# Kernel optimization log

Measured on AMD Instinct MI355X. Metric: run time of the kernel, lower is better.

The kernel has to match this reference:

```python
import jax, jax.numpy as jnp
import numpy as np

B, S, D = 4, 2048, 2048
E = 64           # num_experts
TOPK = 2         # num_experts_per_token


def setup_inputs() -> dict:
    key = jax.random.key(0)
    k1, k2, k3 = jax.random.split(key, 3)
    x_real = jax.random.normal(k1, (B, S, D), dtype=jnp.float32)
    x_imag = jax.random.normal(k2, (B, S, D), dtype=jnp.float32)
    # flax Dense: kernel [in_features, out_features] with lecun_normal-ish scale
    W = jax.random.normal(k3, (2 * D, E), dtype=jnp.float32) / np.sqrt(2.0 * D)
    b = jnp.zeros((E,), dtype=jnp.float32)
    return {"x_real": x_real, "x_imag": x_imag, "W": W, "b": b}


def reference(x_real, x_imag, W, b):
    # amp = |x|, phase = angle(x) for x = x_real + i*x_imag
    amp = jnp.hypot(x_real, x_imag)                 # [B,S,D]
    phase = jnp.arctan2(x_imag, x_real)             # [B,S,D]
    routing_input = jnp.concatenate([amp, phase], axis=-1)  # [B,S,2D]
    scores = jnp.einsum('bsf,fe->bse', routing_input, W) + b  # [B,S,E]
    probs = jax.nn.softmax(scores, axis=-1)
    top_k_probs, top_k_indices = jax.lax.top_k(probs, TOPK)   # [B,S,K]
    top_k_probs = top_k_probs / jnp.sum(top_k_probs, axis=-1, keepdims=True)
    return (top_k_probs, top_k_indices)
```

## Files before the change

### kernel.cpp

```cpp
#include <hip/hip_runtime.h>
#include <math.h>

#define NTOK 8192
#define DD   2048
#define EE   64
#define MTILE 32
#define KSPLIT 2
#define DPER (DD/KSPLIT)
#define DCHUNK 32
#define NCHUNK (DPER/DCHUNK)
#define APAD 8
#define ASTRIDE (64 + APAD)
#define PROB_N (NTOK*2)

typedef __bf16 bf16x8 __attribute__((ext_vector_type(8)));
typedef float  f32x4  __attribute__((ext_vector_type(4)));

__device__ __forceinline__ unsigned short bf16_rne(float x, float& rep) {
    unsigned u = __builtin_bit_cast(unsigned, x);
    unsigned r = u + 0x7FFFu + ((u >> 16) & 1u);
    unsigned short h = (unsigned short)(r >> 16);
    rep = __builtin_bit_cast(float, (unsigned)h << 16);
    return h;
}

__device__ __forceinline__ void split3(float x, unsigned short& h1,
                                       unsigned short& h2, unsigned short& h3) {
    float f1, f2, f3;
    h1 = bf16_rne(x, f1);
    float r1 = x - f1;
    h2 = bf16_rne(r1, f2);
    float r2 = r1 - f2;
    h3 = bf16_rne(r2, f3);
}

__global__ __launch_bounds__(256) void wsplit(const float* __restrict__ W,
                                              unsigned short* __restrict__ Wt) {
    const int g  = blockIdx.x * 256 + threadIdx.x;
    const int f  = g >> 4;
    const int e4 = g & 15;
    const float4 w = *((const float4*)(W + (size_t)f * EE) + e4);
    const float v[4] = {w.x, w.y, w.z, w.w};
    #pragma unroll
    for (int j = 0; j < 4; ++j) {
        unsigned short h1, h2, h3;
        split3(v[j], h1, h2, h3);
        const int e = e4 * 4 + j;
        Wt[((size_t)(0 * EE + e)) * 4096 + f] = h1;
        Wt[((size_t)(1 * EE + e)) * 4096 + f] = h2;
        Wt[((size_t)(2 * EE + e)) * 4096 + f] = h3;
    }
}

__global__ __launch_bounds__(256) void gemm_mfma(
    const float* __restrict__ xr, const float* __restrict__ xi,
    const unsigned short* __restrict__ Wt, float* __restrict__ part)
{
    __shared__ __align__(16) unsigned short As[3][MTILE][ASTRIDE];

    const int bid   = blockIdx.x;
    const int ks    = bid & (KSPLIT - 1);
    const int strip = bid >> 1;
    const int t0    = strip * MTILE;
    const int dbase = ks * DPER;

    const int tid  = threadIdx.x;
    const int lane = tid & 63;
    const int wv   = tid >> 6;
    const int n0   = wv * 16;

    const int stok = tid >> 3;
    const int sf4  = tid & 7;

    const int fm = lane & 15;
    const int fq = lane >> 4;

    f32x4 acc[2][3];
    #pragma unroll
    for (int mt = 0; mt < 2; ++mt)
        #pragma unroll
        for (int g = 0; g < 3; ++g)
            acc[mt][g] = (f32x4){0.f, 0.f, 0.f, 0.f};

    const float* prx = xr + (size_t)(t0 + stok) * DD + dbase + 4 * sf4;
    const float* pix = xi + (size_t)(t0 + stok) * DD + dbase + 4 * sf4;
    float4 vr = *(const float4*)prx;
    float4 vi = *(const float4*)pix;

    const unsigned short* wb = Wt + (size_t)(n0 + fm) * 4096 + 8 * fq;

    for (int c = 0; c < NCHUNK; ++c) {
        const int d0 = dbase + c * DCHUNK;

        bf16x8 bfr[2][3];
        #pragma unroll
        for (int s = 0; s < 3; ++s) {
            bfr[0][s] = *(const bf16x8*)(wb + (size_t)s * (EE * 4096) + d0);
            bfr[1][s] = *(const bf16x8*)(wb + (size_t)s * (EE * 4096) + 2048 + d0);
        }
        const int cn = (c + 1 < NCHUNK) ? (c + 1) : c;
        const float4 nvr = *(const float4*)(prx + cn * DCHUNK);
        const float4 nvi = *(const float4*)(pix + cn * DCHUNK);

        {
            const float ar[4] = {vr.x, vr.y, vr.z, vr.w};
            const float ai[4] = {vi.x, vi.y, vi.z, vi.w};
            ushort4 a1, a2, a3, p1, p2, p3;
            unsigned short* pa1 = (unsigned short*)&a1;
            unsigned short* pa2 = (unsigned short*)&a2;
            unsigned short* pa3 = (unsigned short*)&a3;
            unsigned short* pp1 = (unsigned short*)&p1;
            unsigned short* pp2 = (unsigned short*)&p2;
            unsigned short* pp3 = (unsigned short*)&p3;
            #pragma unroll
            for (int j = 0; j < 4; ++j) {
                const float amp = sqrtf(ar[j] * ar[j] + ai[j] * ai[j]);
                const float ph  = atan2f(ai[j], ar[j]);
                split3(amp, pa1[j], pa2[j], pa3[j]);
                split3(ph,  pp1[j], pp2[j], pp3[j]);
            }
            *(ushort4*)&As[0][stok][4 * sf4]      = a1;
            *(ushort4*)&As[1][stok][4 * sf4]      = a2;
            *(ushort4*)&As[2][stok][4 * sf4]      = a3;
            *(ushort4*)&As[0][stok][32 + 4 * sf4] = p1;
            *(ushort4*)&As[1][stok][32 + 4 * sf4] = p2;
            *(ushort4*)&As[2][stok][32 + 4 * sf4] = p3;
        }
        __syncthreads();

        #pragma unroll
        for (int st = 0; st < 2; ++st) {
            #pragma unroll
            for (int mt = 0; mt < 2; ++mt) {
                const unsigned short* ab = &As[0][mt * 16 + fm][st * 32 + fq * 8];
                const bf16x8 a0 = *(const bf16x8*)(ab);
                const bf16x8 a1 = *(const bf16x8*)(ab + MTILE * ASTRIDE);
                const bf16x8 a2 = *(const bf16x8*)(ab + 2 * MTILE * ASTRIDE);
                acc[mt][0] = __builtin_amdgcn_mfma_f32_16x16x32_bf16(a0, bfr[st][0], acc[mt][0], 0, 0, 0);
                acc[mt][0] = __builtin_amdgcn_mfma_f32_16x16x32_bf16(a1, bfr[st][1], acc[mt][0], 0, 0, 0);
                acc[mt][1] = __builtin_amdgcn_mfma_f32_16x16x32_bf16(a0, bfr[st][1], acc[mt][1], 0, 0, 0);
                acc[mt][1] = __builtin_amdgcn_mfma_f32_16x16x32_bf16(a1, bfr[st][0], acc[mt][1], 0, 0, 0);
                acc[mt][2] = __builtin_amdgcn_mfma_f32_16x16x32_bf16(a0, bfr[st][2], acc[mt][2], 0, 0, 0);
                acc[mt][2] = __builtin_amdgcn_mfma_f32_16x16x32_bf16(a2, bfr[st][0], acc[mt][2], 0, 0, 0);
            }
        }
        __syncthreads();
        vr = nvr; vi = nvi;
    }

    #pragma unroll
    for (int mt = 0; mt < 2; ++mt) {
        const f32x4 s = acc[mt][0] + acc[mt][1] + acc[mt][2];
        float* pb = part + ((size_t)ks * NTOK + t0 + mt * 16) * EE;
        #pragma unroll
        for (int r = 0; r < 4; ++r)
            pb[(size_t)(fq * 4 + r) * EE + n0 + fm] = s[r];
    }
}

__global__ __launch_bounds__(256) void finalize_topk(
    const float* __restrict__ part, const float* __restrict__ bias,
    float* __restrict__ out)
{
    const int tid  = threadIdx.x;
    const int lane = tid & 63;
    const int w    = tid >> 6;
    const int t    = blockIdx.x * 4 + w;

    float s = bias[lane];
    #pragma unroll
    for (int p = 0; p < KSPLIT; ++p)
        s += part[((size_t)p * NTOK + t) * EE + lane];

    float v1 = s, v2 = -INFINITY;
    int   i1 = lane, i2 = 64;

    #pragma unroll
    for (int off = 1; off < 64; off <<= 1) {
        const float ov1 = __shfl_xor(v1, off, 64);
        const int   oi1 = __shfl_xor(i1, off, 64);
        const float ov2 = __shfl_xor(v2, off, 64);
        const int   oi2 = __shfl_xor(i2, off, 64);
        const bool b1 = (ov1 > v1) || (ov1 == v1 && oi1 < i1);
        const float n1 = b1 ? ov1 : v1;  const int ni1 = b1 ? oi1 : i1;
        const float c1 = b1 ? v1  : ov1; const int ci1 = b1 ? i1  : oi1;
        const float c2 = b1 ? ov2 : v2;  const int ci2 = b1 ? oi2 : i2;
        const bool b2 = (c1 > c2) || (c1 == c2 && ci1 < ci2);
        v1 = n1; i1 = ni1;
        v2 = b2 ? c1 : c2; i2 = b2 ? ci1 : ci2;
    }

    if (lane == 0) {
        const float z  = expf(v2 - v1);
        const float p1 = 1.0f / (1.0f + z);
        const float p2 = z / (1.0f + z);
        out[(size_t)t * 2 + 0] = p1;
        out[(size_t)t * 2 + 1] = p2;
        out[PROB_N + (size_t)t * 2 + 0] = (float)i1;
        out[PROB_N + (size_t)t * 2 + 1] = (float)i2;
    }
}

extern "C" void kernel_launch(void* const* d_in, const int* in_sizes, int n_in,
                              void* d_out, int out_size, void* d_ws, size_t ws_size,
                              hipStream_t stream) {
    const float* xr = (const float*)d_in[0];
    const float* xi = (const float*)d_in[1];
    const float* W  = (const float*)d_in[2];
    const float* b  = (const float*)d_in[3];
    float* out = (float*)d_out;

    float* part = (float*)d_ws;
    unsigned short* Wt = (unsigned short*)((char*)d_ws + (size_t)KSPLIT * NTOK * EE * 4);

    wsplit<<<256, 256, 0, stream>>>(W, Wt);
    gemm_mfma<<<(NTOK / MTILE) * KSPLIT, 256, 0, stream>>>(xr, xi, Wt, part);
    finalize_topk<<<NTOK / 4, 256, 0, stream>>>(part, b, out);
}
```

Measured before the change: 195.8 us.

## Drop LDS staging, compute A fragments in registers, split-K 4 with atomics

Each wave now loads its own 16 token rows and builds the amp/phase bf16 split fragments directly in registers, which removes the shared-memory staging and both block barriers. The tile grows to 64 tokens with 4 wave-rows, and each wave covers all 64 experts with 4 accumulators. K is split 4 ways and partial scores are combined with float atomicAdd into a buffer that the wsplit kernel zeroes. This removes the LDS round trip and the partial-sum reads in the finalize kernel. In exchange each wave reloads the full W fragment set with no sharing across waves, more register pressure is accepted, and atomic accumulation makes the summation order nondeterministic.

New measurement: 243.9 us. 1.25x slower.

```diff
diff --git a/kernel.cpp b/kernel.cpp
--- a/kernel.cpp
+++ b/kernel.cpp
@@ -4,17 +4,16 @@
 #define NTOK 8192
 #define DD   2048
 #define EE   64
-#define MTILE 32
-#define KSPLIT 2
+#define KSPLIT 4
 #define DPER (DD/KSPLIT)
-#define DCHUNK 32
-#define NCHUNK (DPER/DCHUNK)
-#define APAD 8
-#define ASTRIDE (64 + APAD)
+#define NCHUNK (DPER/32)
+#define FTOT (2*DD)
+#define WT_SSTRIDE (EE*FTOT)
 #define PROB_N (NTOK*2)
 
 typedef __bf16 bf16x8 __attribute__((ext_vector_type(8)));
 typedef float  f32x4  __attribute__((ext_vector_type(4)));
+typedef unsigned short u16x8 __attribute__((ext_vector_type(8)));
 
 __device__ __forceinline__ unsigned short bf16_rne(float x, float& rep) {
     unsigned u = __builtin_bit_cast(unsigned, x);
@@ -35,131 +34,130 @@
 }
 
 __global__ __launch_bounds__(256) void wsplit(const float* __restrict__ W,
-                                              unsigned short* __restrict__ Wt) {
+                                              unsigned short* __restrict__ Wt,
+                                              float* __restrict__ score) {
     const int g  = blockIdx.x * 256 + threadIdx.x;
-    const int f  = g >> 4;
-    const int e4 = g & 15;
-    const float4 w = *((const float4*)(W + (size_t)f * EE) + e4);
-    const float v[4] = {w.x, w.y, w.z, w.w};
-    #pragma unroll
-    for (int j = 0; j < 4; ++j) {
+    const int e  = g >> 9;
+    const int f0 = (g & 511) * 8;
+    u16x8 h1v, h2v, h3v;
+    #pragma unroll
+    for (int j = 0; j < 8; ++j) {
         unsigned short h1, h2, h3;
-        split3(v[j], h1, h2, h3);
-        const int e = e4 * 4 + j;
-        Wt[((size_t)(0 * EE + e)) * 4096 + f] = h1;
-        Wt[((size_t)(1 * EE + e)) * 4096 + f] = h2;
-        Wt[((size_t)(2 * EE + e)) * 4096 + f] = h3;
-    }
-}
-
-__global__ __launch_bounds__(256) void gemm_mfma(
+        split3(W[(size_t)(f0 + j) * EE + e], h1, h2, h3);
+        h1v[j] = h1; h2v[j] = h2; h3v[j] = h3;
+    }
+    const size_t o = (size_t)e * FTOT + f0;
+    *(u16x8*)&Wt[0 * WT_SSTRIDE + o] = h1v;
+    *(u16x8*)&Wt[1 * WT_SSTRIDE + o] = h2v;
+    *(u16x8*)&Wt[2 * WT_SSTRIDE + o] = h3v;
+
+    float4* sz = (float4*)score;
+    #pragma unroll
+    for (int k = 0; k < 4; ++k)
+        sz[(size_t)g * 4 + k] = make_float4(0.f, 0.f, 0.f, 0.f);
+}
+
+__global__ __launch_bounds__(256, 2) void gemm_mfma(
     const float* __restrict__ xr, const float* __restrict__ xi,
-    const unsigned short* __restrict__ Wt, float* __restrict__ part)
+    const unsigned short* __restrict__ Wt, float* __restrict__ score)
 {
-    __shared__ __align__(16) unsigned short As[3][MTILE][ASTRIDE];
-
     const int bid   = blockIdx.x;
     const int ks    = bid & (KSPLIT - 1);
-    const int strip = bid >> 1;
-    const int t0    = strip * MTILE;
+    const int strip = bid >> 2;
+    const int t0    = strip * 64;
     const int dbase = ks * DPER;
 
     const int tid  = threadIdx.x;
+    const int wv   = tid >> 6;
     const int lane = tid & 63;
-    const int wv   = tid >> 6;
-    const int n0   = wv * 16;
-
-    const int stok = tid >> 3;
-    const int sf4  = tid & 7;
-
-    const int fm = lane & 15;
-    const int fq = lane >> 4;
-
-    f32x4 acc[2][3];
-    #pragma unroll
-    for (int mt = 0; mt < 2; ++mt)
-        #pragma unroll
-        for (int g = 0; g < 3; ++g)
-            acc[mt][g] = (f32x4){0.f, 0.f, 0.f, 0.f};
-
-    const float* prx = xr + (size_t)(t0 + stok) * DD + dbase + 4 * sf4;
-    const float* pix = xi + (size_t)(t0 + stok) * DD + dbase + 4 * sf4;
-    float4 vr = *(const float4*)prx;
-    float4 vi = *(const float4*)pix;
-
-    const unsigned short* wb = Wt + (size_t)(n0 + fm) * 4096 + 8 * fq;
+    const int fm   = lane & 15;
+    const int fq   = lane >> 4;
+
+    const int trow = t0 + wv * 16 + fm;
+    const float* prx = xr + (size_t)trow * DD + dbase + fq * 8;
+    const float* pix = xi + (size_t)trow * DD + dbase + fq * 8;
+    const unsigned short* wb = Wt + (size_t)fm * FTOT + fq * 8;
+
+    f32x4 acc[4];
+    #pragma unroll
+    for (int n = 0; n < 4; ++n) acc[n] = (f32x4){0.f, 0.f, 0.f, 0.f};
+
+    float4 vr0 = *(const float4*)(prx);
+    float4 vr1 = *(const float4*)(prx + 4);
+    float4 vi0 = *(const float4*)(pix);
+    float4 vi1 = *(const float4*)(pix + 4);
 
     for (int c = 0; c < NCHUNK; ++c) {
-        const int d0 = dbase + c * DCHUNK;
-
-        bf16x8 bfr[2][3];
-        #pragma unroll
-        for (int s = 0; s < 3; ++s) {
-            bfr[0][s] = *(const bf16x8*)(wb + (size_t)s * (EE * 4096) + d0);
-            bfr[1][s] = *(const bf16x8*)(wb + (size_t)s * (EE * 4096) + 2048 + d0);
+        const int d0 = dbase + c * 32;
+
+        const int off = ((c + 1 < NCHUNK) ? (c + 1) : c) * 32;
+        const float4 nr0 = *(const float4*)(prx + off);
+        const float4 nr1 = *(const float4*)(prx + off + 4);
+        const float4 ni0 = *(const float4*)(pix + off);
+        const float4 ni1 = *(const float4*)(pix + off + 4);
+
+        bf16x8 ba[4][3], bp[4][3];
+        #pragma unroll
+        for (int n = 0; n < 4; ++n)
+            #pragma unroll
+            for (int s = 0; s < 3; ++s) {
+                const unsigned short* p = wb + (size_t)n * 16 * FTOT + (size_t)s * WT_SSTRIDE + d0;
+                ba[n][s] = *(const bf16x8*)(p);
+                bp[n][s] = *(const bf16x8*)(p + DD);
+            }
+
+        const float ar[8] = {vr0.x, vr0.y, vr0.z, vr0.w, vr1.x, vr1.y, vr1.z, vr1.w};
+        const float ai[8] = {vi0.x, vi0.y, vi0.z, vi0.w, vi1.x, vi1.y, vi1.z, vi1.w};
+        u16x8 ua[3], up[3];
+        #pragma unroll
+        for (int j = 0; j < 8; ++j) {
+            const float amp = sqrtf(fmaf(ar[j], ar[j], ai[j] * ai[j]));
+            const float ph  = atan2f(ai[j], ar[j]);
+            unsigned short h1, h2, h3;
+            split3(amp, h1, h2, h3);
+            ua[0][j] = h1; ua[1][j] = h2; ua[2][j] = h3;
+            split3(ph, h1, h2, h3);
+            up[0][j] = h1; up[1][j] = h2; up[2][j] = h3;
         }
-        const int cn = (c + 1 < NCHUNK) ? (c + 1) : c;
-        const float4 nvr = *(const float4*)(prx + cn * DCHUNK);
-        const float4 nvi = *(const float4*)(pix + cn * DCHUNK);
-
-        {
-            const float ar[4] = {vr.x, vr.y, vr.z, vr.w};
-            const float ai[4] = {vi.x, vi.y, vi.z, vi.w};
-            ushort4 a1, a2, a3, p1, p2, p3;
-            unsigned short* pa1 = (unsigned short*)&a1;
-            unsigned short* pa2 = (unsigned short*)&a2;
-            unsigned short* pa3 = (unsigned short*)&a3;
-            unsigned short* pp1 = (unsigned short*)&p1;
-            unsigned short* pp2 = (unsigned short*)&p2;
-            unsigned short* pp3 = (unsigned short*)&p3;
-            #pragma unroll
-            for (int j = 0; j < 4; ++j) {
-                const float amp = sqrtf(ar[j] * ar[j] + ai[j] * ai[j]);
-                const float ph  = atan2f(ai[j], ar[j]);
-                split3(amp, pa1[j], pa2[j], pa3[j]);
-                split3(ph,  pp1[j], pp2[j], pp3[j]);
-            }
-            *(ushort4*)&As[0][stok][4 * sf4]      = a1;
-            *(ushort4*)&As[1][stok][4 * sf4]      = a2;
-            *(ushort4*)&As[2][stok][4 * sf4]      = a3;
-            *(ushort4*)&As[0][stok][32 + 4 * sf4] = p1;
-            *(ushort4*)&As[1][stok][32 + 4 * sf4] = p2;
-            *(ushort4*)&As[2][stok][32 + 4 * sf4] = p3;
+        const bf16x8 aa0 = __builtin_bit_cast(bf16x8, ua[0]);
+        const bf16x8 aa1 = __builtin_bit_cast(bf16x8, ua[1]);
+        const bf16x8 aa2 = __builtin_bit_cast(bf16x8, ua[2]);
+        const bf16x8 ap0 = __builtin_bit_cast(bf16x8, up[0]);
+        const bf16x8 ap1 = __builtin_bit_cast(bf16x8, up[1]);
+        const bf16x8 ap2 = __builtin_bit_cast(bf16x8, up[2]);
+
+        #pragma unroll
+        for (int n = 0; n < 4; ++n) {
+            acc[n] = __builtin_amdgcn_mfma_f32_16x16x32_bf16(aa0, ba[n][0], acc[n], 0, 0, 0);
+            acc[n] = __builtin_amdgcn_mfma_f32_16x16x32_bf16(aa0, ba[n][1], acc[n], 0, 0, 0);
+            acc[n] = __builtin_amdgcn_mfma_f32_16x16x32_bf16(aa1, ba[n][0], acc[n], 0, 0, 0);
+            acc[n] = __builtin_amdgcn_mfma_f32_16x16x32_bf16(aa0, ba[n][2], acc[n], 0, 0, 0);
+            acc[n] = __builtin_amdgcn_mfma_f32_16x16x32_bf16(aa1, ba[n][1], acc[n], 0, 0, 0);
+            acc[n] = __builtin_amdgcn_mfma_f32_16x16x32_bf16(aa2, ba[n][0], acc[n], 0, 0, 0);
         }
-        __syncthreads();
-
-        #pragma unroll
-        for (int st = 0; st < 2; ++st) {
-            #pragma unroll
-            for (int mt = 0; mt < 2; ++mt) {
-                const unsigned short* ab = &As[0][mt * 16 + fm][st * 32 + fq * 8];
-                const bf16x8 a0 = *(const bf16x8*)(ab);
-                const bf16x8 a1 = *(const bf16x8*)(ab + MTILE * ASTRIDE);
-                const bf16x8 a2 = *(const bf16x8*)(ab + 2 * MTILE * ASTRIDE);
-                acc[mt][0] = __builtin_amdgcn_mfma_f32_16x16x32_bf16(a0, bfr[st][0], acc[mt][0], 0, 0, 0);
-                acc[mt][0] = __builtin_amdgcn_mfma_f32_16x16x32_bf16(a1, bfr[st][1], acc[mt][0], 0, 0, 0);
-                acc[mt][1] = __builtin_amdgcn_mfma_f32_16x16x32_bf16(a0, bfr[st][1], acc[mt][1], 0, 0, 0);
-                acc[mt][1] = __builtin_amdgcn_mfma_f32_16x16x32_bf16(a1, bfr[st][0], acc[mt][1], 0, 0, 0);
-                acc[mt][2] = __builtin_amdgcn_mfma_f32_16x16x32_bf16(a0, bfr[st][2], acc[mt][2], 0, 0, 0);
-                acc[mt][2] = __builtin_amdgcn_mfma_f32_16x16x32_bf16(a2, bfr[st][0], acc[mt][2], 0, 0, 0);
-            }
+        #pragma unroll
+        for (int n = 0; n < 4; ++n) {
+            acc[n] = __builtin_amdgcn_mfma_f32_16x16x32_bf16(ap0, bp[n][0], acc[n], 0, 0, 0);
+            acc[n] = __builtin_amdgcn_mfma_f32_16x16x32_bf16(ap0, bp[n][1], acc[n], 0, 0, 0);
+            acc[n] = __builtin_amdgcn_mfma_f32_16x16x32_bf16(ap1, bp[n][0], acc[n], 0, 0, 0);
+            acc[n] = __builtin_amdgcn_mfma_f32_16x16x32_bf16(ap0, bp[n][2], acc[n], 0, 0, 0);
+            acc[n] = __builtin_amdgcn_mfma_f32_16x16x32_bf16(ap1, bp[n][1], acc[n], 0, 0, 0);
+            acc[n] = __builtin_amdgcn_mfma_f32_16x16x32_bf16(ap2, bp[n][0], acc[n], 0, 0, 0);
         }
-        __syncthreads();
-        vr = nvr; vi = nvi;
-    }
-
-    #pragma unroll
-    for (int mt = 0; mt < 2; ++mt) {
-        const f32x4 s = acc[mt][0] + acc[mt][1] + acc[mt][2];
-        float* pb = part + ((size_t)ks * NTOK + t0 + mt * 16) * EE;
+
+        vr0 = nr0; vr1 = nr1; vi0 = ni0; vi1 = ni1;
+    }
+
+    float* sb = score + (size_t)(t0 + wv * 16 + fq * 4) * EE + fm;
+    #pragma unroll
+    for (int n = 0; n < 4; ++n)
         #pragma unroll
         for (int r = 0; r < 4; ++r)
-            pb[(size_t)(fq * 4 + r) * EE + n0 + fm] = s[r];
-    }
+            atomicAdd(sb + (size_t)r * EE + n * 16, acc[n][r]);
 }
 
 __global__ __launch_bounds__(256) void finalize_topk(
-    const float* __restrict__ part, const float* __restrict__ bias,
+    const float* __restrict__ score, const float* __restrict__ bias,
     float* __restrict__ out)
 {
     const int tid  = threadIdx.x;
@@ -167,10 +165,7 @@
     const int w    = tid >> 6;
     const int t    = blockIdx.x * 4 + w;
 
-    float s = bias[lane];
-    #pragma unroll
-    for (int p = 0; p < KSPLIT; ++p)
-        s += part[((size_t)p * NTOK + t) * EE + lane];
+    float s = bias[lane] + score[(size_t)t * EE + lane];
 
     float v1 = s, v2 = -INFINITY;
     int   i1 = lane, i2 = 64;
@@ -210,10 +205,10 @@
     const float* b  = (const float*)d_in[3];
     float* out = (float*)d_out;
 
-    float* part = (float*)d_ws;
-    unsigned short* Wt = (unsigned short*)((char*)d_ws + (size_t)KSPLIT * NTOK * EE * 4);
-
-    wsplit<<<256, 256, 0, stream>>>(W, Wt);
-    gemm_mfma<<<(NTOK / MTILE) * KSPLIT, 256, 0, stream>>>(xr, xi, Wt, part);
-    finalize_topk<<<NTOK / 4, 256, 0, stream>>>(part, b, out);
-}
+    float* score = (float*)d_ws;
+    unsigned short* Wt = (unsigned short*)((char*)d_ws + (size_t)NTOK * EE * 4);
+
+    wsplit<<<128, 256, 0, stream>>>(W, Wt, score);
+    gemm_mfma<<<(NTOK / 64) * KSPLIT, 256, 0, stream>>>(xr, xi, Wt, score);
+    finalize_topk<<<NTOK / 4, 256, 0, stream>>>(score, b, out);
+}
```
